# Kernel tuning notes

Hardware: AMD Instinct MI355X
Metric: run time of the kernel (lower is better)

The kernel has to match this reference:

```python
import jax, jax.numpy as jnp
import numpy as np

# Multi-scale deformable attention (Deformable-DETR / MMCV MSDA), faithful math.
SHAPES = [(100, 100), (50, 50), (25, 25), (13, 13)]  # (H_l, W_l) per level
B, C, NH, L, P = 2, 256, 8, 4, 4
LV = sum(h * w for h, w in SHAPES)  # 13294
LQ = LV
D = C // NH  # head dim = 32


def setup_inputs() -> dict:
    k = jax.random.split(jax.random.key(0), 10)
    rn = lambda i, sh, sc=1.0: jax.random.normal(k[i], sh, jnp.float32) * sc
    starts = np.cumsum([0] + [h * w for h, w in SHAPES])[:L]
    return {
        "query": rn(0, (LQ, B, C)),
        "reference_points": jax.random.uniform(k[1], (B, LQ, L, 2), jnp.float32),
        "value": rn(2, (LV, B, C)),
        "spatial_shapes": jnp.array(SHAPES, jnp.int32),
        "level_start_index": jnp.array(starts, jnp.int32),
        "Wv": rn(3, (C, C), C ** -0.5), "bv": jnp.zeros((C,), jnp.float32),
        "Woff": rn(4, (C, NH * L * P * 2), 0.01), "boff": rn(5, (NH * L * P * 2,), 0.3),
        "Wattn": rn(6, (C, NH * L * P), 0.02), "battn": jnp.zeros((NH * L * P,), jnp.float32),
        "Wo": rn(7, (C, C), C ** -0.5), "bo": jnp.zeros((C,), jnp.float32),
    }


def _bilinear(v, loc, Hl, Wl):
    """v: [B,NH,Hl*Wl,D]; loc: [B,Lq,NH,P,2] normalized (x,y) in (0,1).
    grid_sample(align_corners=False, padding_mode='zeros') equivalent."""
    x = loc[..., 0] * Wl - 0.5
    y = loc[..., 1] * Hl - 0.5
    x0 = jnp.floor(x); y0 = jnp.floor(y)
    wx = x - x0; wy = y - y0
    x0i = x0.astype(jnp.int32); y0i = y0.astype(jnp.int32)
    lq = loc.shape[1]
    acc = jnp.zeros((B, NH, lq * P, D), v.dtype)
    for dy, wyc in ((0, 1.0 - wy), (1, wy)):
        for dx, wxc in ((0, 1.0 - wx), (1, wx)):
            xi = x0i + dx; yi = y0i + dy
            valid = (xi >= 0) & (xi < Wl) & (yi >= 0) & (yi < Hl)
            idx = jnp.clip(yi, 0, Hl - 1) * Wl + jnp.clip(xi, 0, Wl - 1)  # [B,Lq,NH,P]
            idx2 = jnp.transpose(idx, (0, 2, 1, 3)).reshape(B, NH, lq * P)
            g = jnp.take_along_axis(v, idx2[..., None], axis=2)  # [B,NH,Lq*P,D]
            w = jnp.where(valid, wyc * wxc, 0.0).astype(v.dtype)
            w2 = jnp.transpose(w, (0, 2, 1, 3)).reshape(B, NH, lq * P, 1)
            acc = acc + g * w2
    return acc.reshape(B, NH, lq, P, D)


def _msda(q, rp, v, spatial_shapes, Wv, bv, Woff, boff, Wattn, battn, Wo, bo):
    # q: [B,Lq,C], v: [B,Lv,C] (batch-first), rp: [B,Lq,L,2]
    rp = jnp.clip(rp, 1e-5, 1.0 - 1e-5)  # wrapper clamp
    val = (v @ Wv + bv).reshape(B, LV, NH, D)
    val = jnp.transpose(val, (0, 2, 1, 3))  # [B,NH,Lv,D]
    off = (q @ Woff + boff).reshape(B, LQ, NH, L, P, 2)
    attn = jax.nn.softmax((q @ Wattn + battn).reshape(B, LQ, NH, L * P), axis=-1)
    attn = attn.reshape(B, LQ, NH, L, P)
    ss = spatial_shapes.astype(jnp.float32)
    norm = jnp.stack([ss[:, 1], ss[:, 0]], -1)  # [L,2] = (W_l, H_l)
    loc = rp[:, :, None, :, None, :] + off / norm[None, None, None, :, None, :]
    out = jnp.zeros((B, LQ, NH, D), q.dtype)
    start = 0
    for lvl, (Hl, Wl) in enumerate(SHAPES):
        vl = val[:, :, start:start + Hl * Wl]  # [B,NH,Hl*Wl,D]
        sampled = _bilinear(vl, loc[:, :, :, lvl], Hl, Wl)  # [B,NH,Lq,P,D]
        out = out + jnp.einsum('bhqpd,bqhp->bqhd', sampled, attn[:, :, :, lvl])
        start += Hl * Wl
    out = out.reshape(B, LQ, C) @ Wo + bo
    return out + q  # MMCV residual: dropout(output) + identity (dropout=0 at eval)


def reference(query, reference_points, value, spatial_shapes, level_start_index,
              Wv, bv, Woff, boff, Wattn, battn, Wo, bo):
    q = jnp.swapaxes(query, 0, 1)   # wrapper: seq-first -> batch-first
    v = jnp.swapaxes(value, 0, 1)
    out = _msda(q, reference_points, v, spatial_shapes,
                Wv, bv, Woff, boff, Wattn, battn, Wo, bo)
    return jnp.swapaxes(out, 0, 1)  # back to [Lq,B,C]
```

## Files before the change

### kernel.cpp

```cpp
#include <hip/hip_runtime.h>
#include <math.h>

namespace {

typedef __attribute__((ext_vector_type(8))) short short8;
typedef __attribute__((ext_vector_type(4))) float f32x4;

constexpr int B  = 2;
constexpr int C  = 256;
constexpr int NH = 8;
constexpr int L  = 4;
constexpr int P  = 4;
constexpr int D  = 32;
constexpr int LV = 13294;
constexpr int LQ = 13294;
constexpr int M  = B * LQ;

constexpr int SZ[4]    = {100, 50, 25, 13};
constexpr int START[4] = {0, 10000, 12500, 13125};

constexpr int CVT_BLOCKS = (2 * M) / 4;
constexpr int RS = 264;

__device__ inline short bf16r(float f) {
  unsigned u = __float_as_uint(f);
  u += 0x7fff + ((u >> 16) & 1);
  return (short)(u >> 16);
}

__device__ inline void load_a_bf16(const unsigned short* __restrict__ arow, short8 a[8]) {
#pragma unroll
  for (int s = 0; s < 8; ++s)
    a[s] = *reinterpret_cast<const short8*>(arow + s * 32);
}

__global__ __launch_bounds__(256) void k_pre(
    const float* __restrict__ query, const float* __restrict__ value,
    const float* __restrict__ Wv, const float* __restrict__ Woff,
    const float* __restrict__ Wattn, const float* __restrict__ Wo,
    unsigned short* __restrict__ qbf, unsigned short* __restrict__ vbf,
    unsigned short* __restrict__ Btv, unsigned short* __restrict__ Btoa,
    unsigned short* __restrict__ Bto) {
  __shared__ float tile[32][33];
  if (blockIdx.x < CVT_BLOCKS) {
    const int gid = blockIdx.x * 256 + threadIdx.x;
    const int rid = gid >> 6;
    if (rid >= 2 * M) return;
    const int c4 = (gid & 63) * 4;
    const int tensor = (rid >= M) ? 1 : 0;
    const int m = tensor ? rid - M : rid;
    const int b = m / LQ, i = m - b * LQ;
    const float* src = (tensor ? value : query) + ((size_t)(i * B + b)) * C + c4;
    const f32x4 f = *reinterpret_cast<const f32x4*>(src);
    unsigned short* dst = (tensor ? vbf : qbf) + (size_t)m * C + c4;
    uint2 o;
    o.x = (unsigned)(unsigned short)bf16r(f[0]) | ((unsigned)(unsigned short)bf16r(f[1]) << 16);
    o.y = (unsigned)(unsigned short)bf16r(f[2]) | ((unsigned)(unsigned short)bf16r(f[3]) << 16);
    *reinterpret_cast<uint2*>(dst) = o;
    return;
  }
  const int blk = blockIdx.x - CVT_BLOCKS;
  const float* src; unsigned short* dst; int N, local;
  if (blk < 64)       { src = Wv;    dst = Btv;              N = 256; local = blk; }
  else if (blk < 128) { src = Woff;  dst = Btoa;             N = 256; local = blk - 64; }
  else if (blk < 160) { src = Wattn; dst = Btoa + 256 * 256; N = 128; local = blk - 128; }
  else                { src = Wo;    dst = Bto;              N = 256; local = blk - 160; }
  const int ntiles = N >> 5;
  const int kt = local / ntiles, nt = local - kt * ntiles;
  const int k0 = kt << 5, n0 = nt << 5;
  const int tx = threadIdx.x & 31, ty = threadIdx.x >> 5;
#pragma unroll
  for (int r = 0; r < 4; ++r) {
    const int kk = ty + r * 8;
    tile[kk][tx] = src[(size_t)(k0 + kk) * N + n0 + tx];
  }
  __syncthreads();
#pragma unroll
  for (int r = 0; r < 4; ++r) {
    const int nn = ty + r * 8;
    dst[(size_t)(n0 + nn) * 256 + k0 + tx] = (unsigned short)bf16r(tile[tx][nn]);
  }
}


__global__ __launch_bounds__(256, 2) void k_gemm12(
    const unsigned short* __restrict__ qbf, const unsigned short* __restrict__ vbf,
    const float* __restrict__ rp,
    const unsigned short* __restrict__ Btv, const unsigned short* __restrict__ Btoa,
    const float* __restrict__ bv, const float* __restrict__ boff,
    const float* __restrict__ battn,
    unsigned short* __restrict__ val, float* __restrict__ loc,
    float* __restrict__ attn) {
  __shared__ unsigned short sB[128 * RS];
  const int tid = threadIdx.x;
  const int wave = tid >> 6, lane = tid & 63, quad = lane >> 4, lo = lane & 15;
  const int y = blockIdx.y;
  const bool isval = (y < 2);
  const unsigned short* Abf = isval ? vbf : qbf;
  const unsigned short* Bt  = isval ? Btv : Btoa;
  const int n0 = isval ? y * 128 : (y - 2) * 128;
  const int m0 = blockIdx.x * 128;

#pragma unroll
  for (int i = 0; i < 16; ++i) {
    const int cid = i * 256 + tid;
    const int row = cid >> 5, cc = cid & 31;
    const uint4 v = *reinterpret_cast<const uint4*>(Bt + (((size_t)(n0 + row)) << 8) + cc * 8);
    *reinterpret_cast<uint4*>(&sB[row * RS + cc * 8]) = v;
  }

  const int mrow = m0 + wave * 32;
  short8 a[2][8];
#pragma unroll
  for (int c = 0; c < 2; ++c) {
    const int mr = min(mrow + c * 16 + lo, M - 1);
    load_a_bf16(Abf + (size_t)mr * 256 + quad * 8, a[c]);
  }
  __syncthreads();

#pragma unroll 1
  for (int tt = 0; tt < 8; ++tt) {
    const unsigned short* bsrc = &sB[(tt * 16 + lo) * RS + quad * 8];
    short8 b[8];
#pragma unroll
    for (int s = 0; s < 8; ++s)
      b[s] = *reinterpret_cast<const short8*>(bsrc + s * 32);
    f32x4 acc[2];
    acc[0] = (f32x4){0.f, 0.f, 0.f, 0.f};
    acc[1] = (f32x4){0.f, 0.f, 0.f, 0.f};
#pragma unroll
    for (int s = 0; s < 8; ++s) {
      acc[0] = __builtin_amdgcn_mfma_f32_16x16x32_bf16(b[s], a[0][s], acc[0], 0, 0, 0);
      acc[1] = __builtin_amdgcn_mfma_f32_16x16x32_bf16(b[s], a[1][s], acc[1], 0, 0, 0);
    }

    const int nb = n0 + tt * 16 + quad * 4;
    if (isval) {
      const f32x4 bias4 = *reinterpret_cast<const f32x4*>(bv + nb);
      const int h = nb >> 5, d0 = nb & 31;
#pragma unroll
      for (int c = 0; c < 2; ++c) {
        const int m = mrow + c * 16 + lo;
        if (m < M) {
          const int bb = m / LV, i = m - bb * LV;
          ushort4 o;
          o.x = (unsigned short)bf16r(acc[c][0] + bias4[0]);
          o.y = (unsigned short)bf16r(acc[c][1] + bias4[1]);
          o.z = (unsigned short)bf16r(acc[c][2] + bias4[2]);
          o.w = (unsigned short)bf16r(acc[c][3] + bias4[3]);
          *reinterpret_cast<ushort4*>(
              val + (((size_t)(bb * NH + h)) * LV + i) * D + d0) = o;
        }
      }
    } else if (nb < 256) {
      const f32x4 bias4 = *reinterpret_cast<const f32x4*>(boff + nb);
      const int l = (nb >> 3) & 3;
      const float sz = (l == 0) ? 100.f : (l == 1) ? 50.f : (l == 2) ? 25.f : 13.f;
#pragma unroll
      for (int c = 0; c < 2; ++c) {
        const int m = mrow + c * 16 + lo;
        if (m < M) {
          const float2 rv2 = *reinterpret_cast<const float2*>(rp + (size_t)m * 8 + l * 2);
          const float rx = fminf(fmaxf(rv2.x, 1e-5f), 1.f - 1e-5f);
          const float ry = fminf(fmaxf(rv2.y, 1e-5f), 1.f - 1e-5f);
          f32x4 o;
          o[0] = rx + (acc[c][0] + bias4[0]) / sz;
          o[1] = ry + (acc[c][1] + bias4[1]) / sz;
          o[2] = rx + (acc[c][2] + bias4[2]) / sz;
          o[3] = ry + (acc[c][3] + bias4[3]) / sz;
          *reinterpret_cast<f32x4*>(loc + (size_t)m * 256 + nb) = o;
        }
      }
    } else {
      const int n2 = nb - 256;
      const f32x4 bias4 = *reinterpret_cast<const f32x4*>(battn + n2);
#pragma unroll
      for (int c = 0; c < 2; ++c) {
        float v0 = acc[c][0] + bias4[0], v1 = acc[c][1] + bias4[1];
        float v2 = acc[c][2] + bias4[2], v3 = acc[c][3] + bias4[3];
        float mx = fmaxf(fmaxf(v0, v1), fmaxf(v2, v3));
        mx = fmaxf(mx, __shfl_xor(mx, 16, 64));
        mx = fmaxf(mx, __shfl_xor(mx, 32, 64));
        const float e0 = __expf(v0 - mx), e1 = __expf(v1 - mx);
        const float e2 = __expf(v2 - mx), e3 = __expf(v3 - mx);
        float s = e0 + e1 + e2 + e3;
        s += __shfl_xor(s, 16, 64);
        s += __shfl_xor(s, 32, 64);
        const float inv = 1.f / s;
        const int m = mrow + c * 16 + lo;
        if (m < M) {
          f32x4 o; o[0] = e0 * inv; o[1] = e1 * inv; o[2] = e2 * inv; o[3] = e3 * inv;
          *reinterpret_cast<f32x4*>(attn + (size_t)m * 128 + n2) = o;
        }
      }
    }
  }
}

__global__ __launch_bounds__(256, 2) void k_gemm3(
    const unsigned short* __restrict__ tmp, const float* __restrict__ query,
    const unsigned short* __restrict__ Bt, const float* __restrict__ bo,
    float* __restrict__ out) {
  __shared__ unsigned short sB[128 * RS];
  const int tid = threadIdx.x;
  const int wave = tid >> 6, lane = tid & 63, quad = lane >> 4, lo = lane & 15;
  const int n0 = blockIdx.y * 128;
  const int m0 = blockIdx.x * 128;

#pragma unroll
  for (int i = 0; i < 16; ++i) {
    const int cid = i * 256 + tid;
    const int row = cid >> 5, cc = cid & 31;
    const uint4 v = *reinterpret_cast<const uint4*>(Bt + (((size_t)(n0 + row)) << 8) + cc * 8);
    *reinterpret_cast<uint4*>(&sB[row * RS + cc * 8]) = v;
  }
  const int mrow = m0 + wave * 32;
  short8 a[2][8];
#pragma unroll
  for (int c = 0; c < 2; ++c) {
    const int mr = min(mrow + c * 16 + lo, M - 1);
    load_a_bf16(tmp + (size_t)mr * 256 + quad * 8, a[c]);
  }
  __syncthreads();

#pragma unroll 1
  for (int tt = 0; tt < 8; ++tt) {
    const unsigned short* bsrc = &sB[(tt * 16 + lo) * RS + quad * 8];
    short8 b[8];
#pragma unroll
    for (int s = 0; s < 8; ++s)
      b[s] = *reinterpret_cast<const short8*>(bsrc + s * 32);
    f32x4 acc[2];
    acc[0] = (f32x4){0.f, 0.f, 0.f, 0.f};
    acc[1] = (f32x4){0.f, 0.f, 0.f, 0.f};
#pragma unroll
    for (int s = 0; s < 8; ++s) {
      acc[0] = __builtin_amdgcn_mfma_f32_16x16x32_bf16(b[s], a[0][s], acc[0], 0, 0, 0);
      acc[1] = __builtin_amdgcn_mfma_f32_16x16x32_bf16(b[s], a[1][s], acc[1], 0, 0, 0);
    }
    const int nb = n0 + tt * 16 + quad * 4;
    const f32x4 bias4 = *reinterpret_cast<const f32x4*>(bo + nb);
#pragma unroll
    for (int c = 0; c < 2; ++c) {
      const int m = mrow + c * 16 + lo;
      if (m < M) {
        const int bb = m / LQ, q = m - bb * LQ;
        const size_t o = ((size_t)(q * B + bb)) * C + nb;
        const f32x4 qv = *reinterpret_cast<const f32x4*>(query + o);
        f32x4 ov;
        ov[0] = acc[c][0] + bias4[0] + qv[0];
        ov[1] = acc[c][1] + bias4[1] + qv[1];
        ov[2] = acc[c][2] + bias4[2] + qv[2];
        ov[3] = acc[c][3] + bias4[3] + qv[3];
        *reinterpret_cast<f32x4*>(out + o) = ov;
      }
    }
  }
}

__global__ __launch_bounds__(256, 4) void k_sample(
    const unsigned short* __restrict__ val, const float* __restrict__ loc,
    const float* __restrict__ attn, unsigned short* __restrict__ tmp) {
  constexpr int QPB = 8;
  const int mblk = blockIdx.x * QPB;
  const int t = threadIdx.x;
  __shared__ float sloc[QPB * 8 * 33];
  __shared__ float sattn[QPB * 8 * 17];
  for (int i = t; i < QPB * 256; i += 256) {
    int mq = mblk + (i >> 8); if (mq >= M) mq = M - 1;
    const int j = i & 255;
    sloc[(((i >> 8) << 3) + (j >> 5)) * 33 + (j & 31)] = loc[(size_t)mq * 256 + j];
  }
  for (int i = t; i < QPB * 128; i += 256) {
    int mq = mblk + (i >> 7); if (mq >= M) mq = M - 1;
    const int j = i & 127;
    sattn[(((i >> 7) << 3) + (j >> 4)) * 17 + (j & 15)] = attn[(size_t)mq * 128 + j];
  }
  __syncthreads();

  const int g = t >> 5, s = t & 31, h = s >> 2, c8 = s & 3;
  const int m = mblk + g;
  const int mc = (m < M) ? m : M - 1;
  const int b = mc / LQ;
  const unsigned short* vhead = val + ((size_t)(b * NH + h) * LV) * D + c8 * 8;
  const float* ql = sloc + (g * 8 + h) * 33;
  const float* qa = sattn + (g * 8 + h) * 17;

  float acc[8] = {0.f, 0.f, 0.f, 0.f, 0.f, 0.f, 0.f, 0.f};
#pragma unroll 1
  for (int l = 0; l < L; ++l) {
    const int Wl = SZ[l];
    const float Wlf = (float)Wl;
    const unsigned short* vlev = vhead + (size_t)START[l] * D;
#pragma unroll 2
    for (int p = 0; p < P; ++p) {
      const float x = ql[l * 8 + p * 2]     * Wlf - 0.5f;
      const float y = ql[l * 8 + p * 2 + 1] * Wlf - 0.5f;
      const float aw = qa[l * 4 + p];
      const float x0f = floorf(x), y0f = floorf(y);
      const float wx = x - x0f, wy = y - y0f;
      const int x0 = (int)x0f, y0 = (int)y0f;
      const float wy1 = wy * aw, wy0 = aw - wy1;
      const float wx1 = wx, wx0 = 1.f - wx;
#pragma unroll
      for (int dy = 0; dy < 2; ++dy) {
#pragma unroll
        for (int dx = 0; dx < 2; ++dx) {
          const int yi = y0 + dy, xi = x0 + dx;
          const bool ok = (xi >= 0) & (xi < Wl) & (yi >= 0) & (yi < Wl);
          const int yc = min(max(yi, 0), Wl - 1);
          const int xc = min(max(xi, 0), Wl - 1);
          const float w = ok ? (dy ? wy1 : wy0) * (dx ? wx1 : wx0) : 0.f;
          const uint4 raw = *reinterpret_cast<const uint4*>(vlev + (yc * Wl + xc) * D);
          acc[0] = fmaf(w, __uint_as_float(raw.x << 16),          acc[0]);
          acc[1] = fmaf(w, __uint_as_float(raw.x & 0xffff0000u),  acc[1]);
          acc[2] = fmaf(w, __uint_as_float(raw.y << 16),          acc[2]);
          acc[3] = fmaf(w, __uint_as_float(raw.y & 0xffff0000u),  acc[3]);
          acc[4] = fmaf(w, __uint_as_float(raw.z << 16),          acc[4]);
          acc[5] = fmaf(w, __uint_as_float(raw.z & 0xffff0000u),  acc[5]);
          acc[6] = fmaf(w, __uint_as_float(raw.w << 16),          acc[6]);
          acc[7] = fmaf(w, __uint_as_float(raw.w & 0xffff0000u),  acc[7]);
        }
      }
    }
  }
  if (m < M) {
    short8 o;
#pragma unroll
    for (int j = 0; j < 8; ++j) o[j] = bf16r(acc[j]);
    *reinterpret_cast<short8*>(tmp + (size_t)m * 256 + h * 32 + c8 * 8) = o;
  }
}

}

extern "C" void kernel_launch(void* const* d_in, const int* in_sizes, int n_in,
                              void* d_out, int out_size, void* d_ws, size_t ws_size,
                              hipStream_t stream) {
  const float* query = (const float*)d_in[0];
  const float* rp    = (const float*)d_in[1];
  const float* value = (const float*)d_in[2];
  const float* Wv    = (const float*)d_in[5];
  const float* bv    = (const float*)d_in[6];
  const float* Woff  = (const float*)d_in[7];
  const float* boff  = (const float*)d_in[8];
  const float* Wattn = (const float*)d_in[9];
  const float* battn = (const float*)d_in[10];
  const float* Wo    = (const float*)d_in[11];
  const float* bo    = (const float*)d_in[12];
  float* out = (float*)d_out;

  unsigned short* Btv  = (unsigned short*)d_ws;
  unsigned short* Btoa = Btv + 256 * 256;
  unsigned short* Bto  = Btoa + 384 * 256;
  unsigned short* qbf  = Bto + 256 * 256;
  unsigned short* vbf  = qbf + (size_t)M * 256;
  unsigned short* val  = vbf + (size_t)M * 256;
  float* loc  = (float*)(val + (size_t)M * 256);
  float* attn = loc + (size_t)M * 256;
  unsigned short* tmp = vbf;

  const int mtiles128 = (M + 127) / 128;
  const int sample_blocks = (M + 7) / 8;

  k_pre<<<CVT_BLOCKS + 224, 256, 0, stream>>>(query, value, Wv, Woff, Wattn, Wo,
                                              qbf, vbf, Btv, Btoa, Bto);
  k_gemm12<<<dim3(mtiles128, 5), 256, 0, stream>>>(qbf, vbf, rp, Btv, Btoa,
                                                   bv, boff, battn, val, loc, attn);
  k_sample<<<sample_blocks, 256, 0, stream>>>(val, loc, attn, tmp);
  k_gemm3<<<dim3(mtiles128, 2), 256, 0, stream>>>(tmp, query, Bto, bo, out);
}
```

Measured before the change: 238.3 us.

## Fuse fp32-to-bf16 input conversion into GEMM A-loads and pack sampling FMAs

Removes the separate pass that converted query and value to bf16 in a workspace. The GEMM now reads the fp32 inputs directly, applying the seq-first to batch-first index remap itself and converting with packed v_cvt_pk_bf16_f32 instructions. This drops one full write and read of two M×256 bf16 tensors, but each of the five y-blocks per row tile now re-reads fp32 A rows at twice the bytes. Separately, the sampling kernel hoists the four corner loads and masks, and accumulates in float2 vectors so the compiler can emit packed FMAs.

```diff
diff --git a/kernel.cpp b/kernel.cpp
--- a/kernel.cpp
+++ b/kernel.cpp
@@ -5,6 +5,7 @@
 
 typedef __attribute__((ext_vector_type(8))) short short8;
 typedef __attribute__((ext_vector_type(4))) float f32x4;
+typedef __attribute__((ext_vector_type(2))) float f32x2;
 
 constexpr int B  = 2;
 constexpr int C  = 256;
@@ -19,7 +20,6 @@
 constexpr int SZ[4]    = {100, 50, 25, 13};
 constexpr int START[4] = {0, 10000, 12500, 13125};
 
-constexpr int CVT_BLOCKS = (2 * M) / 4;
 constexpr int RS = 264;
 
 __device__ inline short bf16r(float f) {
@@ -28,6 +28,24 @@
   return (short)(u >> 16);
 }
 
+__device__ inline short8 cvt8(const f32x4 lo, const f32x4 hi) {
+  union { uint4 u; short8 s; } r;
+  asm("v_cvt_pk_bf16_f32 %0, %1, %2" : "=v"(r.u.x) : "v"(lo[0]), "v"(lo[1]));
+  asm("v_cvt_pk_bf16_f32 %0, %1, %2" : "=v"(r.u.y) : "v"(lo[2]), "v"(lo[3]));
+  asm("v_cvt_pk_bf16_f32 %0, %1, %2" : "=v"(r.u.z) : "v"(hi[0]), "v"(hi[1]));
+  asm("v_cvt_pk_bf16_f32 %0, %1, %2" : "=v"(r.u.w) : "v"(hi[2]), "v"(hi[3]));
+  return r.s;
+}
+
+__device__ inline void load_a_cvt(const float* __restrict__ arow, short8 a[8]) {
+#pragma unroll
+  for (int s = 0; s < 8; ++s) {
+    const f32x4 lo = *reinterpret_cast<const f32x4*>(arow + s * 32);
+    const f32x4 hi = *reinterpret_cast<const f32x4*>(arow + s * 32 + 4);
+    a[s] = cvt8(lo, hi);
+  }
+}
+
 __device__ inline void load_a_bf16(const unsigned short* __restrict__ arow, short8 a[8]) {
 #pragma unroll
   for (int s = 0; s < 8; ++s)
@@ -35,31 +53,12 @@
 }
 
 __global__ __launch_bounds__(256) void k_pre(
-    const float* __restrict__ query, const float* __restrict__ value,
     const float* __restrict__ Wv, const float* __restrict__ Woff,
     const float* __restrict__ Wattn, const float* __restrict__ Wo,
-    unsigned short* __restrict__ qbf, unsigned short* __restrict__ vbf,
     unsigned short* __restrict__ Btv, unsigned short* __restrict__ Btoa,
     unsigned short* __restrict__ Bto) {
   __shared__ float tile[32][33];
-  if (blockIdx.x < CVT_BLOCKS) {
-    const int gid = blockIdx.x * 256 + threadIdx.x;
-    const int rid = gid >> 6;
-    if (rid >= 2 * M) return;
-    const int c4 = (gid & 63) * 4;
-    const int tensor = (rid >= M) ? 1 : 0;
-    const int m = tensor ? rid - M : rid;
-    const int b = m / LQ, i = m - b * LQ;
-    const float* src = (tensor ? value : query) + ((size_t)(i * B + b)) * C + c4;
-    const f32x4 f = *reinterpret_cast<const f32x4*>(src);
-    unsigned short* dst = (tensor ? vbf : qbf) + (size_t)m * C + c4;
-    uint2 o;
-    o.x = (unsigned)(unsigned short)bf16r(f[0]) | ((unsigned)(unsigned short)bf16r(f[1]) << 16);
-    o.y = (unsigned)(unsigned short)bf16r(f[2]) | ((unsigned)(unsigned short)bf16r(f[3]) << 16);
-    *reinterpret_cast<uint2*>(dst) = o;
-    return;
-  }
-  const int blk = blockIdx.x - CVT_BLOCKS;
+  const int blk = blockIdx.x;
   const float* src; unsigned short* dst; int N, local;
   if (blk < 64)       { src = Wv;    dst = Btv;              N = 256; local = blk; }
   else if (blk < 128) { src = Woff;  dst = Btoa;             N = 256; local = blk - 64; }
@@ -82,9 +81,8 @@
   }
 }
 
-
 __global__ __launch_bounds__(256, 2) void k_gemm12(
-    const unsigned short* __restrict__ qbf, const unsigned short* __restrict__ vbf,
+    const float* __restrict__ query, const float* __restrict__ value,
     const float* __restrict__ rp,
     const unsigned short* __restrict__ Btv, const unsigned short* __restrict__ Btoa,
     const float* __restrict__ bv, const float* __restrict__ boff,
@@ -96,7 +94,7 @@
   const int wave = tid >> 6, lane = tid & 63, quad = lane >> 4, lo = lane & 15;
   const int y = blockIdx.y;
   const bool isval = (y < 2);
-  const unsigned short* Abf = isval ? vbf : qbf;
+  const float* __restrict__ Af = isval ? value : query;
   const unsigned short* Bt  = isval ? Btv : Btoa;
   const int n0 = isval ? y * 128 : (y - 2) * 128;
   const int m0 = blockIdx.x * 128;
@@ -114,7 +112,8 @@
 #pragma unroll
   for (int c = 0; c < 2; ++c) {
     const int mr = min(mrow + c * 16 + lo, M - 1);
-    load_a_bf16(Abf + (size_t)mr * 256 + quad * 8, a[c]);
+    const int bb = mr / LQ, ii = mr - bb * LQ;
+    load_a_cvt(Af + ((size_t)(ii * 2 + bb)) * 256 + quad * 8, a[c]);
   }
   __syncthreads();
 
@@ -286,7 +285,9 @@
   const float* ql = sloc + (g * 8 + h) * 33;
   const float* qa = sattn + (g * 8 + h) * 17;
 
-  float acc[8] = {0.f, 0.f, 0.f, 0.f, 0.f, 0.f, 0.f, 0.f};
+  f32x2 acc[4];
+  acc[0] = (f32x2){0.f, 0.f}; acc[1] = (f32x2){0.f, 0.f};
+  acc[2] = (f32x2){0.f, 0.f}; acc[3] = (f32x2){0.f, 0.f};
 #pragma unroll 1
   for (int l = 0; l < L; ++l) {
     const int Wl = SZ[l];
@@ -300,34 +301,49 @@
       const float x0f = floorf(x), y0f = floorf(y);
       const float wx = x - x0f, wy = y - y0f;
       const int x0 = (int)x0f, y0 = (int)y0f;
-      const float wy1 = wy * aw, wy0 = aw - wy1;
-      const float wx1 = wx, wx0 = 1.f - wx;
-#pragma unroll
-      for (int dy = 0; dy < 2; ++dy) {
-#pragma unroll
-        for (int dx = 0; dx < 2; ++dx) {
-          const int yi = y0 + dy, xi = x0 + dx;
-          const bool ok = (xi >= 0) & (xi < Wl) & (yi >= 0) & (yi < Wl);
-          const int yc = min(max(yi, 0), Wl - 1);
-          const int xc = min(max(xi, 0), Wl - 1);
-          const float w = ok ? (dy ? wy1 : wy0) * (dx ? wx1 : wx0) : 0.f;
-          const uint4 raw = *reinterpret_cast<const uint4*>(vlev + (yc * Wl + xc) * D);
-          acc[0] = fmaf(w, __uint_as_float(raw.x << 16),          acc[0]);
-          acc[1] = fmaf(w, __uint_as_float(raw.x & 0xffff0000u),  acc[1]);
-          acc[2] = fmaf(w, __uint_as_float(raw.y << 16),          acc[2]);
-          acc[3] = fmaf(w, __uint_as_float(raw.y & 0xffff0000u),  acc[3]);
-          acc[4] = fmaf(w, __uint_as_float(raw.z << 16),          acc[4]);
-          acc[5] = fmaf(w, __uint_as_float(raw.z & 0xffff0000u),  acc[5]);
-          acc[6] = fmaf(w, __uint_as_float(raw.w << 16),          acc[6]);
-          acc[7] = fmaf(w, __uint_as_float(raw.w & 0xffff0000u),  acc[7]);
-        }
+      const int x1 = x0 + 1, y1 = y0 + 1;
+      const float wy1v = wy * aw;
+      const float wy0m = ((unsigned)y0 < (unsigned)Wl) ? (aw - wy1v) : 0.f;
+      const float wy1m = ((unsigned)y1 < (unsigned)Wl) ? wy1v : 0.f;
+      const float wx0m = ((unsigned)x0 < (unsigned)Wl) ? (1.f - wx) : 0.f;
+      const float wx1m = ((unsigned)x1 < (unsigned)Wl) ? wx : 0.f;
+      const int xc0 = min(max(x0, 0), Wl - 1), xc1 = min(max(x1, 0), Wl - 1);
+      const int yc0 = min(max(y0, 0), Wl - 1), yc1 = min(max(y1, 0), Wl - 1);
+      const int r0 = yc0 * Wl, r1 = yc1 * Wl;
+      const uint4 v00 = *reinterpret_cast<const uint4*>(vlev + (r0 + xc0) * D);
+      const uint4 v01 = *reinterpret_cast<const uint4*>(vlev + (r0 + xc1) * D);
+      const uint4 v10 = *reinterpret_cast<const uint4*>(vlev + (r1 + xc0) * D);
+      const uint4 v11 = *reinterpret_cast<const uint4*>(vlev + (r1 + xc1) * D);
+      const float w00 = wy0m * wx0m, w01 = wy0m * wx1m;
+      const float w10 = wy1m * wx0m, w11 = wy1m * wx1m;
+#pragma unroll
+      for (int k = 0; k < 4; ++k) {
+        const uint4 r = (k == 0) ? v00 : (k == 1) ? v01 : (k == 2) ? v10 : v11;
+        const float w = (k == 0) ? w00 : (k == 1) ? w01 : (k == 2) ? w10 : w11;
+        const f32x2 wv = {w, w};
+        f32x2 v;
+        v[0] = __uint_as_float(r.x << 16);
+        v[1] = __uint_as_float(r.x & 0xffff0000u);
+        acc[0] = __builtin_elementwise_fma(v, wv, acc[0]);
+        v[0] = __uint_as_float(r.y << 16);
+        v[1] = __uint_as_float(r.y & 0xffff0000u);
+        acc[1] = __builtin_elementwise_fma(v, wv, acc[1]);
+        v[0] = __uint_as_float(r.z << 16);
+        v[1] = __uint_as_float(r.z & 0xffff0000u);
+        acc[2] = __builtin_elementwise_fma(v, wv, acc[2]);
+        v[0] = __uint_as_float(r.w << 16);
+        v[1] = __uint_as_float(r.w & 0xffff0000u);
+        acc[3] = __builtin_elementwise_fma(v, wv, acc[3]);
       }
     }
   }
   if (m < M) {
     short8 o;
 #pragma unroll
-    for (int j = 0; j < 8; ++j) o[j] = bf16r(acc[j]);
+    for (int j = 0; j < 4; ++j) {
+      o[2 * j]     = bf16r(acc[j][0]);
+      o[2 * j + 1] = bf16r(acc[j][1]);
+    }
     *reinterpret_cast<short8*>(tmp + (size_t)m * 256 + h * 32 + c8 * 8) = o;
   }
 }
@@ -353,19 +369,16 @@
   unsigned short* Btv  = (unsigned short*)d_ws;
   unsigned short* Btoa = Btv + 256 * 256;
   unsigned short* Bto  = Btoa + 384 * 256;
-  unsigned short* qbf  = Bto + 256 * 256;
-  unsigned short* vbf  = qbf + (size_t)M * 256;
-  unsigned short* val  = vbf + (size_t)M * 256;
+  unsigned short* val  = Bto + 256 * 256;
   float* loc  = (float*)(val + (size_t)M * 256);
   float* attn = loc + (size_t)M * 256;
-  unsigned short* tmp = vbf;
+  unsigned short* tmp = (unsigned short*)(attn + (size_t)M * 128);
 
   const int mtiles128 = (M + 127) / 128;
   const int sample_blocks = (M + 7) / 8;
 
-  k_pre<<<CVT_BLOCKS + 224, 256, 0, stream>>>(query, value, Wv, Woff, Wattn, Wo,
-                                              qbf, vbf, Btv, Btoa, Bto);
-  k_gemm12<<<dim3(mtiles128, 5), 256, 0, stream>>>(qbf, vbf, rp, Btv, Btoa,
+  k_pre<<<224, 256, 0, stream>>>(Wv, Woff, Wattn, Wo, Btv, Btoa, Bto);
+  k_gemm12<<<dim3(mtiles128, 5), 256, 0, stream>>>(query, value, rp, Btv, Btoa,
                                                    bv, boff, battn, val, loc, attn);
   k_sample<<<sample_blocks, 256, 0, stream>>>(val, loc, attn, tmp);
   k_gemm3<<<dim3(mtiles128, 2), 256, 0, stream>>>(tmp, query, Bto, bo, out);
```

New measurement: 222.8 us. 6.5% less time.
